# Kernel optimization log

Measured on AMD Instinct MI355X. Metric: run time of the kernel, lower is better.

Reference implementation:

```python
import jax, jax.numpy as jnp
import numpy as np

B, D, N_CLASSES = 8192, 128, 50


def setup_inputs() -> dict:
    key = jax.random.key(0)
    k1, k2, k3 = jax.random.split(key, 3)
    anchor = jax.random.normal(k1, (B, D), dtype=jnp.float32)
    target = jax.random.normal(k2, (B, D), dtype=jnp.float32)
    labels = jax.random.randint(k3, (B,), 0, N_CLASSES)
    return {"anchor": anchor, "target": target, "labels": labels}


def reference(anchor, target, labels):
    # Faithful vectorization of QuadrupletLoss.nt_xent_loss.
    # Note: the original hardcodes temperature 0.05 (ignores self.temp).
    TEMP = 0.05
    n = labels.shape[0]
    diff = labels[:, None] != labels[None, :]                      # mask2: [B,B]
    same_off = (labels[:, None] == labels[None, :]) & ~jnp.eye(n, dtype=bool)  # mask

    # d[j, m] = <anchor[j], target[m]> / 0.05
    d = jnp.matmul(anchor, target.T) / TEMP                        # [B,B]
    neg = jnp.where(diff, d, -jnp.inf)
    mx = jax.lax.stop_gradient(jnp.max(neg, axis=1))               # maxdot.detach() per j
    mx = jnp.where(jnp.isfinite(mx), mx, 0.0)
    # s[j] = sum_{m: labels[m]!=labels[j]} exp(d[j,m] - mx[j])  (exp(-inf)=0 masks out)
    s = jnp.sum(jnp.exp(neg - mx[:, None]), axis=1)                # [B]

    # Inner double loop: nds[i] = sum over j with labels[j]!=labels[i] of s[j]
    difff = diff.astype(s.dtype)
    nds = difff @ s                                                # [B]
    negcount = jnp.sum(difff, axis=1)                              # negtivesum

    x = jnp.where(negcount > 0, nds / jnp.where(negcount > 0, negcount, 1.0), nds)
    log_prob = -jnp.log(x + 1e-12)                                 # constant across cols
    mask_sum = jnp.sum(same_off, axis=1)
    # (mask * log_prob).sum(1) / clamp(mask_sum,1) == log_prob where mask_sum>0 else 0
    pos_logits = jnp.where(mask_sum > 0, log_prob, 0.0)
    return -jnp.mean(pos_logits)
```

## Files before the change

kernel.cpp:

```cpp
#include <hip/hip_runtime.h>
#include <float.h>
#include <math.h>

typedef __attribute__((ext_vector_type(8))) short short8;
typedef __attribute__((ext_vector_type(8))) _Float16 half8;
typedef __attribute__((ext_vector_type(4))) float f32x4;

constexpr int B_N  = 8192;
constexpr int D_KK = 128;
constexpr int NCLS = 50;
constexpr int NCHUNK = 8;
constexpr int BLK_ROWS = 256;
constexpr int TCOLS = 128;
constexpr float C_SCALE   = 28.853900817779268f;
constexpr float MARGIN_DOT = 40.0f / 28.853900817779268f;
constexpr float NEG_LOW  = -1.0e5f;
constexpr float NEG_MASK = -1.0e30f;

__device__ __forceinline__ float exp2fast(float x) { return __builtin_amdgcn_exp2f(x); }

__device__ __forceinline__ void async_copy16(void* lds, const void* g) {
    __builtin_amdgcn_global_load_lds((const __attribute__((address_space(1))) unsigned int*)g,
                                     (__attribute__((address_space(3))) unsigned int*)lds,
                                     16, 0, 0);
}

__global__ void tof16_kernel(const float* __restrict__ a, const float* __restrict__ b,
                             short* __restrict__ aH, short* __restrict__ bH)
{
    const int NPER = B_N * D_KK / 8;
    int i = blockIdx.x * blockDim.x + threadIdx.x;
    const float* src = (i < NPER) ? a : b;
    short*       dst = (i < NPER) ? aH : bH;
    int j = (i < NPER) ? i : i - NPER;
    const f32x4* sp = (const f32x4*)(src + (size_t)j * 8);
    f32x4 v0 = sp[0], v1 = sp[1];
    short8 h;
#pragma unroll
    for (int e = 0; e < 4; ++e) {
        h[e]     = __builtin_bit_cast(short, (_Float16)v0[e]);
        h[e + 4] = __builtin_bit_cast(short, (_Float16)v1[e]);
    }
    *(short8*)(dst + (size_t)j * 8) = h;
}

__global__ __launch_bounds__(512, 2)
void rowstats_kernel(const short* __restrict__ aH, const short* __restrict__ bH,
                     const int* __restrict__ labels,
                     float* __restrict__ pmx, float* __restrict__ ps)
{
    __shared__ __align__(16) char bbuf[2][TCOLS * 256];
    __shared__ float mergebuf[BLK_ROWS][2];

    const int bid   = blockIdx.x;
    const int chunk = bid & (NCHUNK - 1);
    const int R0 = (bid >> 3) * BLK_ROWS;
    const int C0 = chunk * (B_N / NCHUNK);

    const int tid = threadIdx.x;
    const int wid = tid >> 6, l = tid & 63;
    const int l15 = l & 15, l16 = l >> 4;
    const int wr = wid >> 1, wc = wid & 1;

    half8 aF[4][4];
#pragma unroll
    for (int mf = 0; mf < 4; ++mf) {
        const int arow = R0 + wr * 64 + mf * 16 + l15;
#pragma unroll
        for (int ks = 0; ks < 4; ++ks)
            aF[mf][ks] = __builtin_bit_cast(half8,
                *(const short8*)(aH + (size_t)arow * D_KK + ks * 32 + l16 * 8));
    }

    int labA[16];
#pragma unroll
    for (int mf = 0; mf < 4; ++mf)
#pragma unroll
        for (int r = 0; r < 4; ++r)
            labA[mf * 4 + r] = labels[R0 + wr * 64 + mf * 16 + l16 * 4 + r];

    float mx[16], sm[16];
#pragma unroll
    for (int i = 0; i < 16; ++i) { mx[i] = NEG_LOW; sm[i] = 0.0f; }

    const int scol = tid >> 4;
    const int slotp = tid & 15;

    const int NT = (B_N / NCHUNK) / TCOLS;

#define STAGE(tile, bsel)                                                            \
    {                                                                                \
        _Pragma("unroll")                                                            \
        for (int q = 0; q < 4; ++q) {                                                \
            int col = q * 32 + scol;                                                 \
            int gslot = slotp ^ (col & 7);                                           \
            const short* gp = bH + (size_t)(C0 + (tile) * TCOLS + col) * D_KK + gslot * 8; \
            char* lp = &bbuf[bsel][q * 8192 + tid * 16];                             \
            async_copy16(lp, gp);                                                    \
        }                                                                            \
    }

    STAGE(0, 0);
    __syncthreads();

    for (int t = 0; t < NT; ++t) {
        const int cur = t & 1;
        if (t + 1 < NT) STAGE(t + 1, cur ^ 1);

        f32x4 acc[4][4];
#pragma unroll
        for (int mf = 0; mf < 4; ++mf)
#pragma unroll
            for (int nf = 0; nf < 4; ++nf) acc[mf][nf] = f32x4{0.f, 0.f, 0.f, 0.f};

#pragma unroll
        for (int ks = 0; ks < 4; ++ks) {
            half8 bF[4];
#pragma unroll
            for (int nf = 0; nf < 4; ++nf) {
                int col  = wc * 64 + nf * 16 + l15;
                int slot = (ks * 4 + l16) ^ (col & 7);
                bF[nf] = __builtin_bit_cast(half8,
                    *(const short8*)(&bbuf[cur][col * 256 + slot * 16]));
            }
#pragma unroll
            for (int mf = 0; mf < 4; ++mf)
#pragma unroll
                for (int nf = 0; nf < 4; ++nf)
                    acc[mf][nf] = __builtin_amdgcn_mfma_f32_16x16x32_f16(
                        aF[mf][ks], bF[nf], acc[mf][nf], 0, 0, 0);
        }

        const int colB = C0 + t * TCOLS;
        int lB[4];
#pragma unroll
        for (int nf = 0; nf < 4; ++nf) lB[nf] = labels[colB + wc * 64 + nf * 16 + l15];

#pragma unroll
        for (int mf = 0; mf < 4; ++mf) {
            float gm = acc[mf][0][0];
#pragma unroll
            for (int nf = 0; nf < 4; ++nf)
#pragma unroll
                for (int r = 0; r < 4; ++r) gm = fmaxf(gm, acc[mf][nf][r]);
            int sk = 1;
#pragma unroll
            for (int r = 0; r < 4; ++r) sk &= (gm < mx[mf * 4 + r] - MARGIN_DOT) ? 1 : 0;
            if (!__all(sk)) {
#pragma unroll
                for (int r = 0; r < 4; ++r) {
                    const int i = mf * 4 + r;
                    float v0 = (lB[0] != labA[i]) ? acc[mf][0][r] : NEG_MASK;
                    float v1 = (lB[1] != labA[i]) ? acc[mf][1][r] : NEG_MASK;
                    float v2 = (lB[2] != labA[i]) ? acc[mf][2][r] : NEG_MASK;
                    float v3 = (lB[3] != labA[i]) ? acc[mf][3][r] : NEG_MASK;
                    float nm = fmaxf(mx[i], fmaxf(fmaxf(v0, v1), fmaxf(v2, v3)));
                    float e = exp2fast(C_SCALE * (v0 - nm)) + exp2fast(C_SCALE * (v1 - nm))
                            + exp2fast(C_SCALE * (v2 - nm)) + exp2fast(C_SCALE * (v3 - nm));
                    sm[i] = sm[i] * exp2fast(C_SCALE * (mx[i] - nm)) + e;
                    mx[i] = nm;
                }
            }
        }
        __syncthreads();
    }

#pragma unroll
    for (int i = 0; i < 16; ++i) {
#pragma unroll
        for (int off = 1; off < 16; off <<= 1) {
            float m2 = __shfl_xor(mx[i], off);
            float s2 = __shfl_xor(sm[i], off);
            float nm = fmaxf(mx[i], m2);
            sm[i] = sm[i] * exp2fast(C_SCALE * (mx[i] - nm))
                  + s2   * exp2fast(C_SCALE * (m2 - nm));
            mx[i] = nm;
        }
    }

    if (wc == 1 && l15 == 0) {
#pragma unroll
        for (int mf = 0; mf < 4; ++mf)
#pragma unroll
            for (int r = 0; r < 4; ++r) {
                int rl = wr * 64 + mf * 16 + l16 * 4 + r;
                mergebuf[rl][0] = mx[mf * 4 + r];
                mergebuf[rl][1] = sm[mf * 4 + r];
            }
    }
    __syncthreads();
    if (wc == 0 && l15 == 0) {
#pragma unroll
        for (int mf = 0; mf < 4; ++mf)
#pragma unroll
            for (int r = 0; r < 4; ++r) {
                const int i = mf * 4 + r;
                int rl = wr * 64 + mf * 16 + l16 * 4 + r;
                float m2 = mergebuf[rl][0], s2 = mergebuf[rl][1];
                float nm = fmaxf(mx[i], m2);
                float s  = sm[i] * exp2fast(C_SCALE * (mx[i] - nm))
                         + s2   * exp2fast(C_SCALE * (m2 - nm));
                pmx[chunk * B_N + R0 + rl] = nm * C_SCALE;
                ps [chunk * B_N + R0 + rl] = s;
            }
    }
#undef STAGE
}

__global__ void classsum_kernel(const float* __restrict__ pmx, const float* __restrict__ ps,
                                const int* __restrict__ labels,
                                float* __restrict__ classSum, unsigned int* __restrict__ classCnt)
{
    __shared__ float        csL[NCLS];
    __shared__ unsigned int ccL[NCLS];
    int t = threadIdx.x;
    if (t < NCLS) { csL[t] = 0.0f; ccL[t] = 0u; }
    __syncthreads();

    int j = blockIdx.x * blockDim.x + t;
    float m = -FLT_MAX, s = 0.0f;
#pragma unroll
    for (int c = 0; c < NCHUNK; ++c) {
        float m2 = pmx[(size_t)c * B_N + j];
        float s2 = ps [(size_t)c * B_N + j];
        float nm = fmaxf(m, m2);
        s = s * exp2fast(m - nm) + s2 * exp2fast(m2 - nm);
        m = nm;
    }
    int lab = labels[j];
    atomicAdd(&csL[lab], s);
    atomicAdd(&ccL[lab], 1u);
    __syncthreads();
    if (t < NCLS) {
        atomicAdd(&classSum[t], csL[t]);
        atomicAdd(&classCnt[t], ccL[t]);
    }
}

__global__ void loss_kernel(const float* __restrict__ classSum,
                            const unsigned int* __restrict__ classCnt,
                            float* __restrict__ out)
{
    int c = threadIdx.x;
    float cs        = (c < NCLS) ? classSum[c] : 0.0f;
    unsigned int cc = (c < NCLS) ? classCnt[c] : 0u;

    float tot = cs;
#pragma unroll
    for (int off = 1; off < 64; off <<= 1) tot += __shfl_xor(tot, off);

    float contrib = 0.0f;
    if (c < NCLS && cc > 0u) {
        float negc = (float)(B_N - (int)cc);
        float nds  = tot - cs;
        float x    = (negc > 0.0f) ? (nds / negc) : nds;
        float lp   = (cc >= 2u) ? (-logf(x + 1e-12f)) : 0.0f;
        contrib = (float)cc * lp;
    }
#pragma unroll
    for (int off = 1; off < 64; off <<= 1) contrib += __shfl_xor(contrib, off);
    if (c == 0) out[0] = -(contrib / (float)B_N);
}

extern "C" void kernel_launch(void* const* d_in, const int* in_sizes, int n_in,
                              void* d_out, int out_size, void* d_ws, size_t ws_size,
                              hipStream_t stream)
{
    const float* anchor = (const float*)d_in[0];
    const float* target = (const float*)d_in[1];
    const int*   labels = (const int*)d_in[2];
    float* out = (float*)d_out;

    const size_t PLANE = (size_t)B_N * D_KK * sizeof(short);
    char* ws = (char*)d_ws;
    short* aH = (short*)(ws + 0 * PLANE);
    short* bH = (short*)(ws + 1 * PLANE);
    float* ps  = (float*)(ws + 2 * PLANE);
    float* pmx = (float*)(ws + 2 * PLANE + sizeof(float) * NCHUNK * B_N);
    char*  cls = ws + 2 * PLANE + 2 * sizeof(float) * NCHUNK * B_N;
    float*        classSum = (float*)cls;
    unsigned int* classCnt = (unsigned int*)(cls + 256);

    hipMemsetAsync(classSum, 0, 512, stream);

    tof16_kernel<<<2 * (B_N * D_KK / 8) / 256, 256, 0, stream>>>(anchor, target, aH, bH);
    rowstats_kernel<<<(B_N / BLK_ROWS) * NCHUNK, 512, 0, stream>>>(aH, bH, labels, pmx, ps);
    classsum_kernel<<<B_N / 256, 256, 0, stream>>>(pmx, ps, labels, classSum, classCnt);
    loss_kernel<<<1, 64, 0, stream>>>(classSum, classCnt, out);
}
```

Before: 60.78 us.

## Shrink rowstats tiles to 64x64 and fold softmax scale into anchor conversion

The row-statistics kernel is retiled from 256-row blocks of 512 threads with 128-column tiles to 64-row blocks of 256 threads with 64-column tiles. This gives four times as many blocks and fewer registers per wave, aiming for better load balance and occupancy. In exchange, each target tile is reused by fewer rows, which raises L2 traffic. The temperature/log2 scale is now multiplied into the anchor during the fp16 conversion, which drops the per-element scale multiplies in the online-softmax update. That puts larger magnitudes into the fp16 operands.

New measurement: 57.36 us. 5.6% less time.

```diff
diff --git a/kernel.cpp b/kernel.cpp
--- a/kernel.cpp
+++ b/kernel.cpp
@@ -10,10 +10,10 @@
 constexpr int D_KK = 128;
 constexpr int NCLS = 50;
 constexpr int NCHUNK = 8;
-constexpr int BLK_ROWS = 256;
-constexpr int TCOLS = 128;
-constexpr float C_SCALE   = 28.853900817779268f;
-constexpr float MARGIN_DOT = 40.0f / 28.853900817779268f;
+constexpr int BLK_ROWS = 64;
+constexpr int TCOLS = 64;
+constexpr float C_SCALE = 28.853900817779268f;
+constexpr float MARGIN  = 40.0f;
 constexpr float NEG_LOW  = -1.0e5f;
 constexpr float NEG_MASK = -1.0e30f;
 
@@ -32,19 +32,20 @@
     int i = blockIdx.x * blockDim.x + threadIdx.x;
     const float* src = (i < NPER) ? a : b;
     short*       dst = (i < NPER) ? aH : bH;
+    const float  sc  = (i < NPER) ? C_SCALE : 1.0f;
     int j = (i < NPER) ? i : i - NPER;
     const f32x4* sp = (const f32x4*)(src + (size_t)j * 8);
     f32x4 v0 = sp[0], v1 = sp[1];
     short8 h;
 #pragma unroll
     for (int e = 0; e < 4; ++e) {
-        h[e]     = __builtin_bit_cast(short, (_Float16)v0[e]);
-        h[e + 4] = __builtin_bit_cast(short, (_Float16)v1[e]);
+        h[e]     = __builtin_bit_cast(short, (_Float16)(sc * v0[e]));
+        h[e + 4] = __builtin_bit_cast(short, (_Float16)(sc * v1[e]));
     }
     *(short8*)(dst + (size_t)j * 8) = h;
 }
 
-__global__ __launch_bounds__(512, 2)
+__global__ __launch_bounds__(256, 4)
 void rowstats_kernel(const short* __restrict__ aH, const short* __restrict__ bH,
                      const int* __restrict__ labels,
                      float* __restrict__ pmx, float* __restrict__ ps)
@@ -62,29 +63,26 @@
     const int l15 = l & 15, l16 = l >> 4;
     const int wr = wid >> 1, wc = wid & 1;
 
-    half8 aF[4][4];
-#pragma unroll
-    for (int mf = 0; mf < 4; ++mf) {
-        const int arow = R0 + wr * 64 + mf * 16 + l15;
+    half8 aF[2][4];
+#pragma unroll
+    for (int mf = 0; mf < 2; ++mf) {
+        const int arow = R0 + wr * 32 + mf * 16 + l15;
 #pragma unroll
         for (int ks = 0; ks < 4; ++ks)
             aF[mf][ks] = __builtin_bit_cast(half8,
                 *(const short8*)(aH + (size_t)arow * D_KK + ks * 32 + l16 * 8));
     }
 
-    int labA[16];
-#pragma unroll
-    for (int mf = 0; mf < 4; ++mf)
+    int labA[8];
+#pragma unroll
+    for (int mf = 0; mf < 2; ++mf)
 #pragma unroll
         for (int r = 0; r < 4; ++r)
-            labA[mf * 4 + r] = labels[R0 + wr * 64 + mf * 16 + l16 * 4 + r];
-
-    float mx[16], sm[16];
-#pragma unroll
-    for (int i = 0; i < 16; ++i) { mx[i] = NEG_LOW; sm[i] = 0.0f; }
-
-    const int scol = tid >> 4;
-    const int slotp = tid & 15;
+            labA[mf * 4 + r] = labels[R0 + wr * 32 + mf * 16 + l16 * 4 + r];
+
+    float mx[8], sm[8];
+#pragma unroll
+    for (int i = 0; i < 8; ++i) { mx[i] = NEG_LOW; sm[i] = 0.0f; }
 
     const int NT = (B_N / NCHUNK) / TCOLS;
 
@@ -92,10 +90,10 @@
     {                                                                                \
         _Pragma("unroll")                                                            \
         for (int q = 0; q < 4; ++q) {                                                \
-            int col = q * 32 + scol;                                                 \
-            int gslot = slotp ^ (col & 7);                                           \
+            int col = q * 16 + (tid >> 4);                                           \
+            int gslot = (tid & 15) ^ (col & 7);                                      \
             const short* gp = bH + (size_t)(C0 + (tile) * TCOLS + col) * D_KK + gslot * 8; \
-            char* lp = &bbuf[bsel][q * 8192 + tid * 16];                             \
+            char* lp = &bbuf[bsel][q * 4096 + tid * 16];                             \
             async_copy16(lp, gp);                                                    \
         }                                                                            \
     }
@@ -107,57 +105,53 @@
         const int cur = t & 1;
         if (t + 1 < NT) STAGE(t + 1, cur ^ 1);
 
-        f32x4 acc[4][4];
-#pragma unroll
-        for (int mf = 0; mf < 4; ++mf)
-#pragma unroll
-            for (int nf = 0; nf < 4; ++nf) acc[mf][nf] = f32x4{0.f, 0.f, 0.f, 0.f};
+        f32x4 acc[2][2];
+#pragma unroll
+        for (int mf = 0; mf < 2; ++mf)
+#pragma unroll
+            for (int nf = 0; nf < 2; ++nf) acc[mf][nf] = f32x4{0.f, 0.f, 0.f, 0.f};
 
 #pragma unroll
         for (int ks = 0; ks < 4; ++ks) {
-            half8 bF[4];
-#pragma unroll
-            for (int nf = 0; nf < 4; ++nf) {
-                int col  = wc * 64 + nf * 16 + l15;
+            half8 bF[2];
+#pragma unroll
+            for (int nf = 0; nf < 2; ++nf) {
+                int col  = wc * 32 + nf * 16 + l15;
                 int slot = (ks * 4 + l16) ^ (col & 7);
                 bF[nf] = __builtin_bit_cast(half8,
                     *(const short8*)(&bbuf[cur][col * 256 + slot * 16]));
             }
 #pragma unroll
-            for (int mf = 0; mf < 4; ++mf)
-#pragma unroll
-                for (int nf = 0; nf < 4; ++nf)
+            for (int mf = 0; mf < 2; ++mf)
+#pragma unroll
+                for (int nf = 0; nf < 2; ++nf)
                     acc[mf][nf] = __builtin_amdgcn_mfma_f32_16x16x32_f16(
                         aF[mf][ks], bF[nf], acc[mf][nf], 0, 0, 0);
         }
 
         const int colB = C0 + t * TCOLS;
-        int lB[4];
-#pragma unroll
-        for (int nf = 0; nf < 4; ++nf) lB[nf] = labels[colB + wc * 64 + nf * 16 + l15];
-
-#pragma unroll
-        for (int mf = 0; mf < 4; ++mf) {
-            float gm = acc[mf][0][0];
-#pragma unroll
-            for (int nf = 0; nf < 4; ++nf)
-#pragma unroll
-                for (int r = 0; r < 4; ++r) gm = fmaxf(gm, acc[mf][nf][r]);
+        int lB[2];
+#pragma unroll
+        for (int nf = 0; nf < 2; ++nf) lB[nf] = labels[colB + wc * 32 + nf * 16 + l15];
+
+#pragma unroll
+        for (int mf = 0; mf < 2; ++mf) {
+            float gm = fmaxf(fmaxf(fmaxf(acc[mf][0][0], acc[mf][0][1]),
+                                   fmaxf(acc[mf][0][2], acc[mf][0][3])),
+                             fmaxf(fmaxf(acc[mf][1][0], acc[mf][1][1]),
+                                   fmaxf(acc[mf][1][2], acc[mf][1][3])));
             int sk = 1;
 #pragma unroll
-            for (int r = 0; r < 4; ++r) sk &= (gm < mx[mf * 4 + r] - MARGIN_DOT) ? 1 : 0;
+            for (int r = 0; r < 4; ++r) sk &= (gm < mx[mf * 4 + r] - MARGIN) ? 1 : 0;
             if (!__all(sk)) {
 #pragma unroll
                 for (int r = 0; r < 4; ++r) {
                     const int i = mf * 4 + r;
                     float v0 = (lB[0] != labA[i]) ? acc[mf][0][r] : NEG_MASK;
                     float v1 = (lB[1] != labA[i]) ? acc[mf][1][r] : NEG_MASK;
-                    float v2 = (lB[2] != labA[i]) ? acc[mf][2][r] : NEG_MASK;
-                    float v3 = (lB[3] != labA[i]) ? acc[mf][3][r] : NEG_MASK;
-                    float nm = fmaxf(mx[i], fmaxf(fmaxf(v0, v1), fmaxf(v2, v3)));
-                    float e = exp2fast(C_SCALE * (v0 - nm)) + exp2fast(C_SCALE * (v1 - nm))
-                            + exp2fast(C_SCALE * (v2 - nm)) + exp2fast(C_SCALE * (v3 - nm));
-                    sm[i] = sm[i] * exp2fast(C_SCALE * (mx[i] - nm)) + e;
+                    float nm = fmaxf(mx[i], fmaxf(v0, v1));
+                    float e  = exp2fast(v0 - nm) + exp2fast(v1 - nm);
+                    sm[i] = sm[i] * exp2fast(mx[i] - nm) + e;
                     mx[i] = nm;
                 }
             }
@@ -166,24 +160,23 @@
     }
 
 #pragma unroll
-    for (int i = 0; i < 16; ++i) {
+    for (int i = 0; i < 8; ++i) {
 #pragma unroll
         for (int off = 1; off < 16; off <<= 1) {
             float m2 = __shfl_xor(mx[i], off);
             float s2 = __shfl_xor(sm[i], off);
             float nm = fmaxf(mx[i], m2);
-            sm[i] = sm[i] * exp2fast(C_SCALE * (mx[i] - nm))
-                  + s2   * exp2fast(C_SCALE * (m2 - nm));
+            sm[i] = sm[i] * exp2fast(mx[i] - nm) + s2 * exp2fast(m2 - nm);
             mx[i] = nm;
         }
     }
 
     if (wc == 1 && l15 == 0) {
 #pragma unroll
-        for (int mf = 0; mf < 4; ++mf)
+        for (int mf = 0; mf < 2; ++mf)
 #pragma unroll
             for (int r = 0; r < 4; ++r) {
-                int rl = wr * 64 + mf * 16 + l16 * 4 + r;
+                int rl = wr * 32 + mf * 16 + l16 * 4 + r;
                 mergebuf[rl][0] = mx[mf * 4 + r];
                 mergebuf[rl][1] = sm[mf * 4 + r];
             }
@@ -191,16 +184,15 @@
     __syncthreads();
     if (wc == 0 && l15 == 0) {
 #pragma unroll
-        for (int mf = 0; mf < 4; ++mf)
+        for (int mf = 0; mf < 2; ++mf)
 #pragma unroll
             for (int r = 0; r < 4; ++r) {
                 const int i = mf * 4 + r;
-                int rl = wr * 64 + mf * 16 + l16 * 4 + r;
+                int rl = wr * 32 + mf * 16 + l16 * 4 + r;
                 float m2 = mergebuf[rl][0], s2 = mergebuf[rl][1];
                 float nm = fmaxf(mx[i], m2);
-                float s  = sm[i] * exp2fast(C_SCALE * (mx[i] - nm))
-                         + s2   * exp2fast(C_SCALE * (m2 - nm));
-                pmx[chunk * B_N + R0 + rl] = nm * C_SCALE;
+                float s  = sm[i] * exp2fast(mx[i] - nm) + s2 * exp2fast(m2 - nm);
+                pmx[chunk * B_N + R0 + rl] = nm;
                 ps [chunk * B_N + R0 + rl] = s;
             }
     }
@@ -284,7 +276,7 @@
     hipMemsetAsync(classSum, 0, 512, stream);
 
     tof16_kernel<<<2 * (B_N * D_KK / 8) / 256, 256, 0, stream>>>(anchor, target, aH, bH);
-    rowstats_kernel<<<(B_N / BLK_ROWS) * NCHUNK, 512, 0, stream>>>(aH, bH, labels, pmx, ps);
+    rowstats_kernel<<<(B_N / BLK_ROWS) * NCHUNK, 256, 0, stream>>>(aH, bH, labels, pmx, ps);
     classsum_kernel<<<B_N / 256, 256, 0, stream>>>(pmx, ps, labels, classSum, classCnt);
     loss_kernel<<<1, 64, 0, stream>>>(classSum, classCnt, out);
 }
```
